# Kernel optimization log

Hardware: AMD Instinct MI355X
Metric: run time of the kernel (lower is better)

The kernel has to match this reference:

```python
import jax, jax.numpy as jnp
import numpy as np

H, HD = 8, 64  # num_heads, head_dim
EPS = 1e-6

def rmsnorm(x, scale):
    return x * jax.lax.rsqrt(jnp.mean(x * x, axis=-1, keepdims=True) + EPS) * scale

def lecun(key, shape):
    fan_in = shape[0]
    return jax.random.normal(key, shape, dtype=jnp.float32) * (fan_in ** -0.5)

def setup_inputs() -> dict:
    key = jax.random.key(0)
    ks = jax.random.split(key, 12)
    B, S, D = 2, 512, 512
    hidden = H * HD            # 512
    ffn = 4 * D                # 2048
    return {
        "inputs": jax.random.normal(ks[0], (B, S, D), dtype=jnp.float32),
        "mask": jnp.zeros((B, S), dtype=jnp.float32),
        "carry": jnp.zeros((B, H, HD, HD), dtype=jnp.float32),
        "ln1": jnp.ones((D,), dtype=jnp.float32),
        "Wq": lecun(ks[1], (D, hidden)),
        "Wk": lecun(ks[2], (D, hidden)),
        "Wv": lecun(ks[3], (D, hidden)),
        "attn_ln": jnp.ones((hidden,), dtype=jnp.float32),
        "Wo": lecun(ks[4], (hidden, D)),
        "bo": jnp.zeros((D,), dtype=jnp.float32),
        "ln2": jnp.ones((D,), dtype=jnp.float32),
        "Wg": lecun(ks[5], (D, ffn)),
        "Wu": lecun(ks[6], (D, ffn)),
        "Wd": lecun(ks[7], (ffn, D)),
    }

def reference(inputs, mask, carry, ln1, Wq, Wk, Wv, attn_ln, Wo, bo, ln2, Wg, Wu, Wd):
    B, S, D = inputs.shape
    skip = inputs
    x = rmsnorm(inputs, ln1)
    # projections + relu feature map
    q = jax.nn.relu((x @ Wq).reshape(B, S, H, HD))
    k = jax.nn.relu((x @ Wk).reshape(B, S, H, HD))
    v = (x @ Wv).reshape(B, S, H, HD)
    # matrix-valued state update: Bmat_t = v_t k_t^T  [B,S,H,HD,HD]
    Bmat = v[..., :, None] * k[..., None, :]
    # decay: identity, zeroed where mask==1 (episode reset)
    m = mask[:, :, None, None, None]
    A = jnp.broadcast_to(jnp.eye(HD, dtype=x.dtype), Bmat.shape) * (1.0 - m)

    def binop(lhs, rhs):
        a_i, b_i = lhs
        a_j, b_j = rhs
        return jnp.matmul(a_i, a_j), jnp.matmul(b_i, a_j) + b_j

    cum_decay, hidden_states = jax.lax.associative_scan(binop, (A, Bmat), axis=1)
    # fold in incoming carry
    states = jnp.matmul(carry[:, None], cum_decay) + hidden_states  # [B,S,H,HD,HD]
    attn = jnp.matmul(states, q[..., None]).squeeze(-1).reshape(B, S, H * HD)
    attn = rmsnorm(attn, attn_ln)
    y = attn @ Wo + bo
    final_carry = states[:, -1]
    # residual + SwiGLU FFN
    x = y + skip
    skip2 = x
    x = rmsnorm(x, ln2)
    x = (jax.nn.silu(x @ Wg) * (x @ Wu)) @ Wd
    return (final_carry, x + skip2)
```

## Files before the change

### kernel.cpp

```cpp
#include <hip/hip_runtime.h>
#include <math.h>

typedef __bf16 bf16x8 __attribute__((ext_vector_type(8)));
typedef float  f32x4  __attribute__((ext_vector_type(4)));

constexpr int B_=2, S_=512, D_=512, H_=8, HD_=64, FFN_=2048, NC_=8;
constexpr float EPS_=1e-6f;

__device__ __forceinline__ __bf16 f2bf(float f){
    union{float f;unsigned u;}x; x.f=f;
    unsigned r=(x.u+0x7fffu+((x.u>>16)&1u))>>16;
    union{unsigned short s;__bf16 b;}y; y.s=(unsigned short)r; return y.b;
}
__device__ __forceinline__ float bf2f(unsigned short s){
    union{unsigned u;float f;}x; x.u=((unsigned)s)<<16; return x.f;
}
__device__ __forceinline__ void bf8_f32(uint4 p, float* o){
    unsigned w[4]={p.x,p.y,p.z,p.w};
#pragma unroll
    for(int i=0;i<4;i++){ o[2*i]=bf2f((unsigned short)(w[i]&0xffffu)); o[2*i+1]=bf2f((unsigned short)(w[i]>>16)); }
}
__device__ __forceinline__ f32x4 MF(bf16x8 a, bf16x8 b, f32x4 c){
    return __builtin_amdgcn_mfma_f32_16x16x32_bf16(a,b,c,0,0,0);
}
#define GLOAD16(g,l) __builtin_amdgcn_global_load_lds((__attribute__((address_space(1))) const void*)(g),(__attribute__((address_space(3))) void*)(l),16,0,0)

__global__ __launch_bounds__(256) void wprep_k(const float* __restrict__ Wg,
    const float* __restrict__ Wu, const float* __restrict__ Wd,
    const float* __restrict__ Wq, const float* __restrict__ Wk,
    const float* __restrict__ Wv, const float* __restrict__ Wo,
    __bf16* __restrict__ WT){
    int t = blockIdx.x;
    const float* src; __bf16* dst; int K,N,lt;
    if      (t<256){ src=Wg; dst=WT;          K=512;  N=2048; lt=t; }
    else if (t<512){ src=Wu; dst=WT+1048576;  K=512;  N=2048; lt=t-256; }
    else if (t<768){ src=Wd; dst=WT+2097152;  K=2048; N=512;  lt=t-512; }
    else if (t<832){ src=Wq; dst=WT+3145728;  K=512;  N=512;  lt=t-768; }
    else if (t<896){ src=Wk; dst=WT+3407872;  K=512;  N=512;  lt=t-832; }
    else if (t<960){ src=Wv; dst=WT+3670016;  K=512;  N=512;  lt=t-896; }
    else           { src=Wo; dst=WT+3932160;  K=512;  N=512;  lt=t-960; }
    int nt64 = N>>6, tk = lt/nt64, tn = lt%nt64;
    __shared__ __bf16 s[64][72];
    int tid = threadIdx.x;
    {
        int jk = tid>>2, jn0 = (tid&3)*16;
        const float* p = src + (size_t)(tk*64+jk)*N + tn*64 + jn0;
        float4 a0=((const float4*)p)[0], a1=((const float4*)p)[1],
               a2=((const float4*)p)[2], a3=((const float4*)p)[3];
        bf16x8 w0, w1;
        w0[0]=f2bf(a0.x); w0[1]=f2bf(a0.y); w0[2]=f2bf(a0.z); w0[3]=f2bf(a0.w);
        w0[4]=f2bf(a1.x); w0[5]=f2bf(a1.y); w0[6]=f2bf(a1.z); w0[7]=f2bf(a1.w);
        w1[0]=f2bf(a2.x); w1[1]=f2bf(a2.y); w1[2]=f2bf(a2.z); w1[3]=f2bf(a2.w);
        w1[4]=f2bf(a3.x); w1[5]=f2bf(a3.y); w1[6]=f2bf(a3.z); w1[7]=f2bf(a3.w);
        *(bf16x8*)&s[jk][jn0] = w0; *(bf16x8*)&s[jk][jn0+8] = w1;
    }
    __syncthreads();
    {
        int jn = tid>>2, jk0 = (tid&3)*16;
        bf16x8 w0, w1;
#pragma unroll
        for(int j=0;j<8;j++){ w0[j]=s[jk0+j][jn]; w1[j]=s[jk0+8+j][jn]; }
        __bf16* q = dst + (size_t)(tn*64+jn)*K + tk*64 + jk0;
        *(bf16x8*)q = w0; *(bf16x8*)(q+8) = w1;
    }
}

__global__ __launch_bounds__(256) void rowrms_f32_k(const float* __restrict__ X, float* __restrict__ rs){
    int row = blockIdx.x*4 + (threadIdx.x>>6), lane = threadIdx.x&63;
    const float4* p = (const float4*)(X + (size_t)row*D_) + lane*2;
    float4 a=p[0], b=p[1];
    float ss = a.x*a.x+a.y*a.y+a.z*a.z+a.w*a.w + b.x*b.x+b.y*b.y+b.z*b.z+b.w*b.w;
    for(int off=32; off>0; off>>=1) ss += __shfl_down(ss, off, 64);
    if(lane==0) rs[row] = rsqrtf(ss/(float)D_ + EPS_);
}
__global__ __launch_bounds__(256) void rowrms_bf16_k(const __bf16* __restrict__ X, float* __restrict__ rs){
    int row = blockIdx.x*4 + (threadIdx.x>>6), lane = threadIdx.x&63;
    uint4 p = *(const uint4*)(X + (size_t)row*D_ + lane*8);
    float v[8]; bf8_f32(p, v);
    float ss = 0.f;
#pragma unroll
    for(int i=0;i<8;i++) ss += v[i]*v[i];
    for(int off=32; off>0; off>>=1) ss += __shfl_down(ss, off, 64);
    if(lane==0) rs[row] = rsqrtf(ss/(float)D_ + EPS_);
}

__device__ __forceinline__ void stageB_async(const __bf16* __restrict__ Bt, int n0, int K, int kk,
                                             __bf16* sB0, __bf16* sB1, int wave, int lane){
    int row = (wave<<4) + (lane>>2), kq = (lane&3)<<3;
    const __bf16* g = Bt + (size_t)(n0+row)*K + kk + kq;
    GLOAD16(g,      sB0 + (wave<<9));
    GLOAD16(g + 32, sB1 + (wave<<9));
}
__device__ __forceinline__ void stageA_rms_f32(const float* __restrict__ A, const float* __restrict__ rs,
        const float* __restrict__ g, int m0, int K, int kk, __bf16* sA0, __bf16* sA1, int tid){
    int row = tid>>2, kq = (tid&3)<<4;
    float r = rs[m0+row];
    const float4* p = (const float4*)(A + (size_t)(m0+row)*K + kk + kq);
    const float4* gp = (const float4*)(g + kk + kq);
    float4 a[4] = {p[0],p[1],p[2],p[3]};
    float4 gg[4] = {gp[0],gp[1],gp[2],gp[3]};
    bf16x8 w0, w1;
    w0[0]=f2bf(a[0].x*r*gg[0].x); w0[1]=f2bf(a[0].y*r*gg[0].y);
    w0[2]=f2bf(a[0].z*r*gg[0].z); w0[3]=f2bf(a[0].w*r*gg[0].w);
    w0[4]=f2bf(a[1].x*r*gg[1].x); w0[5]=f2bf(a[1].y*r*gg[1].y);
    w0[6]=f2bf(a[1].z*r*gg[1].z); w0[7]=f2bf(a[1].w*r*gg[1].w);
    w1[0]=f2bf(a[2].x*r*gg[2].x); w1[1]=f2bf(a[2].y*r*gg[2].y);
    w1[2]=f2bf(a[2].z*r*gg[2].z); w1[3]=f2bf(a[2].w*r*gg[2].w);
    w1[4]=f2bf(a[3].x*r*gg[3].x); w1[5]=f2bf(a[3].y*r*gg[3].y);
    w1[6]=f2bf(a[3].z*r*gg[3].z); w1[7]=f2bf(a[3].w*r*gg[3].w);
    __bf16* d = (kq<32) ? (sA0 + row*32 + kq) : (sA1 + row*32 + kq-32);
    *(bf16x8*)d = w0; *(bf16x8*)(d+8) = w1;
}
__device__ __forceinline__ void stageA_rms_bf16(const __bf16* __restrict__ A, const float* __restrict__ rs,
        const float* __restrict__ g, int m0, int K, int kk, __bf16* sA0, __bf16* sA1, int tid){
    int row = tid>>2, kq = (tid&3)<<4;
    float r = rs[m0+row];
    const __bf16* p = A + (size_t)(m0+row)*K + kk + kq;
    float v[16]; bf8_f32(*(const uint4*)p, v); bf8_f32(*(const uint4*)(p+8), v+8);
    const float4* gp = (const float4*)(g + kk + kq);
    float4 gg[4] = {gp[0],gp[1],gp[2],gp[3]};
    float gf[16] = {gg[0].x,gg[0].y,gg[0].z,gg[0].w, gg[1].x,gg[1].y,gg[1].z,gg[1].w,
                    gg[2].x,gg[2].y,gg[2].z,gg[2].w, gg[3].x,gg[3].y,gg[3].z,gg[3].w};
    bf16x8 w0, w1;
#pragma unroll
    for(int j=0;j<8;j++){ w0[j]=f2bf(v[j]*r*gf[j]); w1[j]=f2bf(v[8+j]*r*gf[8+j]); }
    __bf16* d = (kq<32) ? (sA0 + row*32 + kq) : (sA1 + row*32 + kq-32);
    *(bf16x8*)d = w0; *(bf16x8*)(d+8) = w1;
}
__device__ __forceinline__ void mfma_tile(const __bf16* sA0, const __bf16* sA1,
        const __bf16* sB0, const __bf16* sB1, int wave, int lane, f32x4 acc[4]){
    int ar = (((wave<<4)+(lane&15))<<5) + ((lane>>4)<<3);
    bf16x8 a0 = *(const bf16x8*)(sA0+ar);
    bf16x8 a1 = *(const bf16x8*)(sA1+ar);
#pragma unroll
    for(int nt=0;nt<4;nt++){
        int br = (((nt<<4)+(lane&15))<<5) + ((lane>>4)<<3);
        acc[nt] = MF(a0, *(const bf16x8*)(sB0+br), acc[nt]);
        acc[nt] = MF(a1, *(const bf16x8*)(sB1+br), acc[nt]);
    }
}

__global__ __launch_bounds__(256) void gemm_qkv_k(const float* __restrict__ in,
        const float* __restrict__ rs1, const float* __restrict__ ln1,
        const __bf16* __restrict__ Bt, __bf16* __restrict__ Qb,
        __bf16* __restrict__ Kb, __bf16* __restrict__ Vb){
    __shared__ __bf16 sA0[2048], sA1[2048], sB0[2048], sB1[2048];
    int tid=threadIdx.x, wave=tid>>6, lane=tid&63;
    int n0 = blockIdx.x*64, m0 = blockIdx.y*64;
    f32x4 acc[4] = {};
    for(int kk=0; kk<512; kk+=64){
        stageB_async(Bt, n0, 512, kk, sB0, sB1, wave, lane);
        stageA_rms_f32(in, rs1, ln1, m0, 512, kk, sA0, sA1, tid);
        __syncthreads();
        mfma_tile(sA0,sA1,sB0,sB1,wave,lane,acc);
        __syncthreads();
    }
    int seg = n0>>9, nc = n0&511;
    __bf16* Out = seg==0 ? Qb : (seg==1 ? Kb : Vb);
    bool rl = seg<2;
    int r0 = (wave<<4) + ((lane>>4)<<2);
#pragma unroll
    for(int nt=0;nt<4;nt++){
        int col = nc + nt*16 + (lane&15);
#pragma unroll
        for(int r=0;r<4;r++){
            float v = acc[nt][r]; if(rl) v = fmaxf(v,0.f);
            Out[(size_t)(m0+r0+r)*512 + col] = f2bf(v);
        }
    }
}

__global__ __launch_bounds__(256) void gemm_wo_k(const __bf16* __restrict__ attn,
        const float* __restrict__ rs2, const float* __restrict__ aln,
        const __bf16* __restrict__ Bt, const float* __restrict__ bo,
        const float* __restrict__ skip, float* __restrict__ outx, __bf16* __restrict__ X1){
    __shared__ __bf16 sA0[2048], sA1[2048], sB0[2048], sB1[2048];
    int tid=threadIdx.x, wave=tid>>6, lane=tid&63;
    int n0 = blockIdx.x*64, m0 = blockIdx.y*64;
    f32x4 acc[4] = {};
    for(int kk=0; kk<512; kk+=64){
        stageB_async(Bt, n0, 512, kk, sB0, sB1, wave, lane);
        stageA_rms_bf16(attn, rs2, aln, m0, 512, kk, sA0, sA1, tid);
        __syncthreads();
        mfma_tile(sA0,sA1,sB0,sB1,wave,lane,acc);
        __syncthreads();
    }
    int r0 = (wave<<4) + ((lane>>4)<<2);
#pragma unroll
    for(int nt=0;nt<4;nt++){
        int col = n0 + nt*16 + (lane&15);
#pragma unroll
        for(int r=0;r<4;r++){
            int row = m0+r0+r;
            float v = acc[nt][r] + bo[col] + skip[(size_t)row*512+col];
            outx[(size_t)row*512+col] = v;
            X1[(size_t)row*512+col] = f2bf(v);
        }
    }
}

__global__ __launch_bounds__(256) void gemm_dual_k(const __bf16* __restrict__ X1,
        const float* __restrict__ rs3, const float* __restrict__ ln2,
        const __bf16* __restrict__ Gt, const __bf16* __restrict__ Ut,
        __bf16* __restrict__ Hb){
    __shared__ __bf16 sA0[2048], sA1[2048], sG0[2048], sG1[2048], sU0[2048], sU1[2048];
    int tid=threadIdx.x, wave=tid>>6, lane=tid&63;
    int n0 = blockIdx.x*64, m0 = blockIdx.y*64;
    f32x4 ag[4] = {}, au[4] = {};
    for(int kk=0; kk<512; kk+=64){
        stageB_async(Gt, n0, 512, kk, sG0, sG1, wave, lane);
        stageB_async(Ut, n0, 512, kk, sU0, sU1, wave, lane);
        stageA_rms_bf16(X1, rs3, ln2, m0, 512, kk, sA0, sA1, tid);
        __syncthreads();
        {
            int ar = (((wave<<4)+(lane&15))<<5) + ((lane>>4)<<3);
            bf16x8 a0 = *(const bf16x8*)(sA0+ar);
            bf16x8 a1 = *(const bf16x8*)(sA1+ar);
#pragma unroll
            for(int nt=0;nt<4;nt++){
                int br = (((nt<<4)+(lane&15))<<5) + ((lane>>4)<<3);
                ag[nt] = MF(a0, *(const bf16x8*)(sG0+br), ag[nt]);
                ag[nt] = MF(a1, *(const bf16x8*)(sG1+br), ag[nt]);
                au[nt] = MF(a0, *(const bf16x8*)(sU0+br), au[nt]);
                au[nt] = MF(a1, *(const bf16x8*)(sU1+br), au[nt]);
            }
        }
        __syncthreads();
    }
    int r0 = (wave<<4) + ((lane>>4)<<2);
#pragma unroll
    for(int nt=0;nt<4;nt++){
        int col = n0 + nt*16 + (lane&15);
#pragma unroll
        for(int r=0;r<4;r++){
            float gv = ag[nt][r], uv = au[nt][r];
            float hv = (gv / (1.f + __expf(-gv))) * uv;
            Hb[(size_t)(m0+r0+r)*FFN_ + col] = f2bf(hv);
        }
    }
}

__global__ __launch_bounds__(256) void gemm_wd_k(const __bf16* __restrict__ Hb,
        const __bf16* __restrict__ Bt, float* __restrict__ outx){
    __shared__ __bf16 sA0[2048], sA1[2048], sB0[2048], sB1[2048];
    int tid=threadIdx.x, wave=tid>>6, lane=tid&63;
    int n0 = blockIdx.x*64, m0 = blockIdx.y*64, ks = blockIdx.z*512;
    f32x4 acc[4] = {};
    int row = (wave<<4) + (lane>>2), kq = (lane&3)<<3;
    for(int kk=ks; kk<ks+512; kk+=64){
        stageB_async(Bt, n0, FFN_, kk, sB0, sB1, wave, lane);
        const __bf16* g = Hb + (size_t)(m0+row)*FFN_ + kk + kq;
        GLOAD16(g,      sA0 + (wave<<9));
        GLOAD16(g + 32, sA1 + (wave<<9));
        __syncthreads();
        mfma_tile(sA0,sA1,sB0,sB1,wave,lane,acc);
        __syncthreads();
    }
    int r0 = (wave<<4) + ((lane>>4)<<2);
#pragma unroll
    for(int nt=0;nt<4;nt++){
        int col = n0 + nt*16 + (lane&15);
#pragma unroll
        for(int r=0;r<4;r++)
            atomicAdd(&outx[(size_t)(m0+r0+r)*512 + col], acc[nt][r]);
    }
}

__global__ __launch_bounds__(256) void scanA_k(const __bf16* __restrict__ Kb,
        const __bf16* __restrict__ Vb, const float* __restrict__ mask,
        __bf16* __restrict__ MS, float* __restrict__ Pws){
    int bid = blockIdx.x;
    int c = bid&7, h = (bid>>3)&7, b = bid>>6;
    __shared__ __bf16 sKT0[2048], sKT1[2048], sVT0[2048], sVT1[2048];
    __shared__ float scv[64], ssp[64];
    int tid = threadIdx.x, wave = tid>>6, lane = tid&63;
    const __bf16* Kg = Kb + (size_t)(b*512 + c*64)*512 + h*64;
    const __bf16* Vg = Vb + (size_t)(b*512 + c*64)*512 + h*64;
    if(tid<64) scv[tid] = 1.f - mask[b*512 + c*64 + tid];
    __syncthreads();
    if(tid==0){
        float sp = 1.f;
        for(int t=63;t>=0;--t){ ssp[t]=sp; sp*=scv[t]; }
        Pws[bid] = sp;
    }
    __syncthreads();
#pragma unroll
    for(int p=0;p<2;p++){
        int t = (tid>>3) + p*32, i0 = (tid&7)*8;
        uint4 kr = *(const uint4*)(Kg + (size_t)t*512 + i0);
        uint4 vr = *(const uint4*)(Vg + (size_t)t*512 + i0);
        const __bf16* kp = (const __bf16*)&kr;
        const unsigned short* vp = (const unsigned short*)&vr;
        float sp = ssp[t];
        __bf16* kh = p ? sKT1 : sKT0;
        __bf16* vh = p ? sVT1 : sVT0;
#pragma unroll
        for(int j=0;j<8;j++){
            kh[(i0+j)*32 + (t&31)] = kp[j];
            vh[(i0+j)*32 + (t&31)] = f2bf(bf2f(vp[j])*sp);
        }
    }
    __syncthreads();
    f32x4 am[4] = {};
    mfma_tile(sVT0, sVT1, sKT0, sKT1, wave, lane, am);
    __bf16* Mo = MS + (size_t)bid*4096;
    int r0 = (wave<<4) + ((lane>>4)<<2);
#pragma unroll
    for(int nt=0;nt<4;nt++){
        int j = nt*16 + (lane&15);
#pragma unroll
        for(int r=0;r<4;r++) Mo[(size_t)(r0+r)*64 + j] = f2bf(am[nt][r]);
    }
}

__global__ __launch_bounds__(256) void scanB_k(const float* __restrict__ carry,
        __bf16* __restrict__ MS, const float* __restrict__ Pws,
        float* __restrict__ carry_out){
    int bh = blockIdx.x, tid = threadIdx.x;
    int i = tid>>2, j0 = (tid&3)*16;
    float s[16];
    const float* ci = carry + (size_t)bh*4096 + i*64 + j0;
    for(int j=0;j<16;j++) s[j]=ci[j];
    for(int cc=0; cc<NC_; ++cc){
        __bf16* p = MS + ((size_t)bh*NC_+cc)*4096 + i*64 + j0;
        float P = Pws[bh*NC_+cc];
        for(int j=0;j<16;j++){
            float m = bf2f(*(const unsigned short*)&p[j]);
            p[j] = f2bf(s[j]);
            s[j] = s[j]*P + m;
        }
    }
    float* co = carry_out + (size_t)bh*4096 + i*64 + j0;
    for(int j=0;j<16;j++) co[j]=s[j];
}

__global__ __launch_bounds__(256) void scanC_k(const __bf16* __restrict__ Qb,
        const __bf16* __restrict__ Kb, const __bf16* __restrict__ Vb,
        const float* __restrict__ mask, const __bf16* __restrict__ MS,
        __bf16* __restrict__ attn){
    int bid = blockIdx.x;
    int c = bid&7, h = (bid>>3)&7, b = bid>>6;
    __shared__ __bf16 sQ0[2048], sQ1[2048], sK0[2048], sK1[2048];
    __shared__ __bf16 sS0[2048], sS1[2048];
    __shared__ __bf16 sVT0[2048], sVT1[2048];
    __shared__ __bf16 sW0[2048], sW1[2048];
    __shared__ float Wtab[64][64];
    __shared__ float scv[64], pp[64];
    int tid = threadIdx.x, wave = tid>>6, lane = tid&63;
    const __bf16* Qg = Qb + (size_t)(b*512 + c*64)*512 + h*64;
    const __bf16* Kg = Kb + (size_t)(b*512 + c*64)*512 + h*64;
    const __bf16* Vg = Vb + (size_t)(b*512 + c*64)*512 + h*64;
    const __bf16* Sg = MS + ((size_t)((b*H_+h)*NC_ + c))*4096;

    stageB_async(Qg, 0, 512, 0, sQ0, sQ1, wave, lane);
    stageB_async(Kg, 0, 512, 0, sK0, sK1, wave, lane);
    stageB_async(Sg, 0, 64,  0, sS0, sS1, wave, lane);
    if(tid<64) scv[tid] = 1.f - mask[b*512 + c*64 + tid];
#pragma unroll
    for(int p=0;p<2;p++){
        int u = (tid>>3) + p*32, i0 = (tid&7)*8;
        uint4 vr = *(const uint4*)(Vg + (size_t)u*512 + i0);
        const __bf16* vp = (const __bf16*)&vr;
        __bf16* vh = p ? sVT1 : sVT0;
#pragma unroll
        for(int j=0;j<8;j++) vh[(i0+j)*32 + (u&31)] = vp[j];
    }
    __syncthreads();
    if(tid<64){
        int u = tid; float w = 1.f;
        for(int t=0;t<64;t++){
            if(t>u) w *= scv[t];
            Wtab[u][t] = (t<u) ? 0.f : w;
        }
    }
    if(tid==64){
        float p=1.f;
        for(int t=0;t<64;t++){ p*=scv[t]; pp[t]=p; }
    }
    f32x4 sc[4] = {};
    mfma_tile(sK0, sK1, sQ0, sQ1, wave, lane, sc);
    __syncthreads();
    {
        int u0 = (wave<<4) + ((lane>>4)<<2);
#pragma unroll
        for(int nt=0;nt<4;nt++){
            int t = nt*16 + (lane&15);
#pragma unroll
            for(int r=0;r<4;r++){
                int u = u0 + r;
                float v = sc[nt][r] * Wtab[u][t];
                ((u<32) ? sW0 : sW1)[t*32 + (u&31)] = f2bf(v);
            }
        }
    }
    __syncthreads();
    f32x4 aI[4] = {}, aX[4] = {};
    mfma_tile(sW0, sW1, sVT0, sVT1, wave, lane, aI);
    mfma_tile(sQ0, sQ1, sS0, sS1, wave, lane, aX);
    int t0 = (wave<<4) + ((lane>>4)<<2);
#pragma unroll
    for(int nt=0;nt<4;nt++){
        int i = nt*16 + (lane&15);
#pragma unroll
        for(int r=0;r<4;r++){
            int t = t0 + r;
            float o = aI[nt][r] + aX[nt][r]*pp[t];
            attn[(size_t)(b*512 + c*64 + t)*512 + h*64 + i] = f2bf(o);
        }
    }
}

extern "C" void kernel_launch(void* const* d_in, const int* in_sizes, int n_in,
                              void* d_out, int out_size, void* d_ws, size_t ws_size,
                              hipStream_t stream) {
    const float* inputs  = (const float*)d_in[0];
    const float* mask    = (const float*)d_in[1];
    const float* carry   = (const float*)d_in[2];
    const float* ln1     = (const float*)d_in[3];
    const float* Wq      = (const float*)d_in[4];
    const float* Wk      = (const float*)d_in[5];
    const float* Wv      = (const float*)d_in[6];
    const float* attn_ln = (const float*)d_in[7];
    const float* Wo      = (const float*)d_in[8];
    const float* bo      = (const float*)d_in[9];
    const float* ln2     = (const float*)d_in[10];
    const float* Wg      = (const float*)d_in[11];
    const float* Wu      = (const float*)d_in[12];
    const float* Wd      = (const float*)d_in[13];

    float* out_carry = (float*)d_out;
    float* out_x     = (float*)d_out + 65536;

    __bf16* wb = (__bf16*)d_ws;
    float*  wf = (float*)d_ws;
    __bf16* WgT   = wb;
    __bf16* WuT   = wb + 1048576;
    __bf16* WdT   = wb + 2097152;
    __bf16* WqkvT = wb + 3145728;
    __bf16* WoT   = wb + 3932160;
    __bf16* Qb    = wb + 4194304;
    __bf16* Kb    = wb + 4718592;
    __bf16* Vb    = wb + 5242880;
    __bf16* Hb    = wb + 3145728;
    __bf16* MS    = wb + 5767168;
    float*  Pws   = wf + 3145728;
    float*  rs1   = wf + 3145856;
    float*  rs2   = wf + 3146880;
    float*  rs3   = wf + 3147904;

    wprep_k<<<dim3(1024), dim3(256), 0, stream>>>(Wg,Wu,Wd,Wq,Wk,Wv,Wo, wb);
    rowrms_f32_k<<<dim3(256), dim3(256), 0, stream>>>(inputs, rs1);
    gemm_qkv_k<<<dim3(24,16), dim3(256), 0, stream>>>(inputs, rs1, ln1, WqkvT, Qb, Kb, Vb);
    scanA_k<<<dim3(128), dim3(256), 0, stream>>>(Kb, Vb, mask, MS, Pws);
    scanB_k<<<dim3(16), dim3(256), 0, stream>>>(carry, MS, Pws, out_carry);
    scanC_k<<<dim3(128), dim3(256), 0, stream>>>(Qb, Kb, Vb, mask, MS, Qb);
    rowrms_bf16_k<<<dim3(256), dim3(256), 0, stream>>>(Qb, rs2);
    gemm_wo_k<<<dim3(8,16), dim3(256), 0, stream>>>(Qb, rs2, attn_ln, WoT, bo, inputs, out_x, Vb);
    rowrms_bf16_k<<<dim3(256), dim3(256), 0, stream>>>(Vb, rs3);
    gemm_dual_k<<<dim3(32,16), dim3(256), 0, stream>>>(Vb, rs3, ln2, WgT, WuT, Hb);
    gemm_wd_k<<<dim3(8,16,4), dim3(256), 0, stream>>>(Hb, WdT, out_x);
}
```

Before: 166.0 us.

## Fuse RMS reductions into GEMM epilogues, merge scan stages, widen GEMM N tiles

Removes the standalone row-RMS kernels. rs1 is now computed inside the weight-prep launch, while rs2 and rs3 are built from sum-of-squares atomics in the scanC and Wo epilogues. The sequential scanB carry-propagation kernel is folded into scanC: each chunk block recomputes its prefix state from earlier chunk summaries and the last chunk writes the final carry. All GEMMs widen their N tile from 64 to 128. This cuts four launches but halves grid sizes, which may lower occupancy on a large GPU, and it adds atomics plus redundant prefix work in scanC.

```diff
diff --git a/kernel.cpp b/kernel.cpp
--- a/kernel.cpp
+++ b/kernel.cpp
@@ -25,12 +25,38 @@
 }
 #define GLOAD16(g,l) __builtin_amdgcn_global_load_lds((__attribute__((address_space(1))) const void*)(g),(__attribute__((address_space(3))) void*)(l),16,0,0)
 
-__global__ __launch_bounds__(256) void wprep_k(const float* __restrict__ Wg,
+__device__ __forceinline__ void rowsq_atomic(float* accb, int row0, int lane, float p[4]){
+#pragma unroll
+    for(int r=0;r<4;r++){
+        float v = p[r];
+        v += __shfl_xor(v, 1, 64);
+        v += __shfl_xor(v, 2, 64);
+        v += __shfl_xor(v, 4, 64);
+        v += __shfl_xor(v, 8, 64);
+        if((lane&15)==0) atomicAdd(accb + row0 + r, v);
+    }
+}
+
+__global__ __launch_bounds__(256) void prep_k(const float* __restrict__ Wg,
     const float* __restrict__ Wu, const float* __restrict__ Wd,
     const float* __restrict__ Wq, const float* __restrict__ Wk,
     const float* __restrict__ Wv, const float* __restrict__ Wo,
-    __bf16* __restrict__ WT){
-    int t = blockIdx.x;
+    __bf16* __restrict__ WT, const float* __restrict__ inputs,
+    float* __restrict__ rs1, float* __restrict__ rs2acc, float* __restrict__ rs3acc){
+    __shared__ __bf16 s[64][72];
+    int t = blockIdx.x, tid = threadIdx.x;
+    if(t >= 1024){
+        int row = (t-1024)*4 + (tid>>6), lane = tid&63;
+        const float4* p = (const float4*)(inputs + (size_t)row*D_) + lane*2;
+        float4 a=p[0], b=p[1];
+        float ss = a.x*a.x+a.y*a.y+a.z*a.z+a.w*a.w + b.x*b.x+b.y*b.y+b.z*b.z+b.w*b.w;
+        for(int off=32; off>0; off>>=1) ss += __shfl_down(ss, off, 64);
+        if(lane==0) rs1[row] = rsqrtf(ss/(float)D_ + EPS_);
+        float4 z = {0.f,0.f,0.f,0.f};
+        if(t==1024) ((float4*)rs2acc)[tid] = z;
+        if(t==1025) ((float4*)rs3acc)[tid] = z;
+        return;
+    }
     const float* src; __bf16* dst; int K,N,lt;
     if      (t<256){ src=Wg; dst=WT;          K=512;  N=2048; lt=t; }
     else if (t<512){ src=Wu; dst=WT+1048576;  K=512;  N=2048; lt=t-256; }
@@ -40,8 +66,6 @@
     else if (t<960){ src=Wv; dst=WT+3670016;  K=512;  N=512;  lt=t-896; }
     else           { src=Wo; dst=WT+3932160;  K=512;  N=512;  lt=t-960; }
     int nt64 = N>>6, tk = lt/nt64, tn = lt%nt64;
-    __shared__ __bf16 s[64][72];
-    int tid = threadIdx.x;
     {
         int jk = tid>>2, jn0 = (tid&3)*16;
         const float* p = src + (size_t)(tk*64+jk)*N + tn*64 + jn0;
@@ -65,27 +89,18 @@
     }
 }
 
-__global__ __launch_bounds__(256) void rowrms_f32_k(const float* __restrict__ X, float* __restrict__ rs){
-    int row = blockIdx.x*4 + (threadIdx.x>>6), lane = threadIdx.x&63;
-    const float4* p = (const float4*)(X + (size_t)row*D_) + lane*2;
-    float4 a=p[0], b=p[1];
-    float ss = a.x*a.x+a.y*a.y+a.z*a.z+a.w*a.w + b.x*b.x+b.y*b.y+b.z*b.z+b.w*b.w;
-    for(int off=32; off>0; off>>=1) ss += __shfl_down(ss, off, 64);
-    if(lane==0) rs[row] = rsqrtf(ss/(float)D_ + EPS_);
-}
-__global__ __launch_bounds__(256) void rowrms_bf16_k(const __bf16* __restrict__ X, float* __restrict__ rs){
-    int row = blockIdx.x*4 + (threadIdx.x>>6), lane = threadIdx.x&63;
-    uint4 p = *(const uint4*)(X + (size_t)row*D_ + lane*8);
-    float v[8]; bf8_f32(p, v);
-    float ss = 0.f;
-#pragma unroll
-    for(int i=0;i<8;i++) ss += v[i]*v[i];
-    for(int off=32; off>0; off>>=1) ss += __shfl_down(ss, off, 64);
-    if(lane==0) rs[row] = rsqrtf(ss/(float)D_ + EPS_);
-}
-
-__device__ __forceinline__ void stageB_async(const __bf16* __restrict__ Bt, int n0, int K, int kk,
-                                             __bf16* sB0, __bf16* sB1, int wave, int lane){
+__device__ __forceinline__ void stageB2(const __bf16* __restrict__ Bt, int n0, int K, int kk,
+                                        __bf16* sB0, __bf16* sB1, int wave, int lane){
+    int row = (wave<<4) + (lane>>2), kq = (lane&3)<<3;
+    const __bf16* g = Bt + (size_t)(n0+row)*K + kk + kq;
+    GLOAD16(g,      sB0 + (wave<<9));
+    GLOAD16(g + 32, sB1 + (wave<<9));
+    const __bf16* g2 = g + (size_t)64*K;
+    GLOAD16(g2,      sB0 + 2048 + (wave<<9));
+    GLOAD16(g2 + 32, sB1 + 2048 + (wave<<9));
+}
+__device__ __forceinline__ void stageB1(const __bf16* __restrict__ Bt, int n0, int K, int kk,
+                                        __bf16* sB0, __bf16* sB1, int wave, int lane){
     int row = (wave<<4) + (lane>>2), kq = (lane&3)<<3;
     const __bf16* g = Bt + (size_t)(n0+row)*K + kk + kq;
     GLOAD16(g,      sB0 + (wave<<9));
@@ -111,10 +126,10 @@
     __bf16* d = (kq<32) ? (sA0 + row*32 + kq) : (sA1 + row*32 + kq-32);
     *(bf16x8*)d = w0; *(bf16x8*)(d+8) = w1;
 }
-__device__ __forceinline__ void stageA_rms_bf16(const __bf16* __restrict__ A, const float* __restrict__ rs,
+__device__ __forceinline__ void stageA_rms_acc(const __bf16* __restrict__ A, const float* __restrict__ ssq,
         const float* __restrict__ g, int m0, int K, int kk, __bf16* sA0, __bf16* sA1, int tid){
     int row = tid>>2, kq = (tid&3)<<4;
-    float r = rs[m0+row];
+    float r = rsqrtf(ssq[m0+row]*(1.f/(float)D_) + EPS_);
     const __bf16* p = A + (size_t)(m0+row)*K + kk + kq;
     float v[16]; bf8_f32(*(const uint4*)p, v); bf8_f32(*(const uint4*)(p+8), v+8);
     const float4* gp = (const float4*)(g + kk + kq);
@@ -139,20 +154,32 @@
         acc[nt] = MF(a1, *(const bf16x8*)(sB1+br), acc[nt]);
     }
 }
+__device__ __forceinline__ void mfma_tile8(const __bf16* sA0, const __bf16* sA1,
+        const __bf16* sB0, const __bf16* sB1, int wave, int lane, f32x4 acc[8]){
+    int ar = (((wave<<4)+(lane&15))<<5) + ((lane>>4)<<3);
+    bf16x8 a0 = *(const bf16x8*)(sA0+ar);
+    bf16x8 a1 = *(const bf16x8*)(sA1+ar);
+#pragma unroll
+    for(int nt=0;nt<8;nt++){
+        int br = (((nt<<4)+(lane&15))<<5) + ((lane>>4)<<3);
+        acc[nt] = MF(a0, *(const bf16x8*)(sB0+br), acc[nt]);
+        acc[nt] = MF(a1, *(const bf16x8*)(sB1+br), acc[nt]);
+    }
+}
 
 __global__ __launch_bounds__(256) void gemm_qkv_k(const float* __restrict__ in,
         const float* __restrict__ rs1, const float* __restrict__ ln1,
         const __bf16* __restrict__ Bt, __bf16* __restrict__ Qb,
         __bf16* __restrict__ Kb, __bf16* __restrict__ Vb){
-    __shared__ __bf16 sA0[2048], sA1[2048], sB0[2048], sB1[2048];
+    __shared__ __bf16 sA0[2048], sA1[2048], sB0[4096], sB1[4096];
     int tid=threadIdx.x, wave=tid>>6, lane=tid&63;
-    int n0 = blockIdx.x*64, m0 = blockIdx.y*64;
-    f32x4 acc[4] = {};
+    int n0 = blockIdx.x*128, m0 = blockIdx.y*64;
+    f32x4 acc[8] = {};
     for(int kk=0; kk<512; kk+=64){
-        stageB_async(Bt, n0, 512, kk, sB0, sB1, wave, lane);
+        stageB2(Bt, n0, 512, kk, sB0, sB1, wave, lane);
         stageA_rms_f32(in, rs1, ln1, m0, 512, kk, sA0, sA1, tid);
         __syncthreads();
-        mfma_tile(sA0,sA1,sB0,sB1,wave,lane,acc);
+        mfma_tile8(sA0,sA1,sB0,sB1,wave,lane,acc);
         __syncthreads();
     }
     int seg = n0>>9, nc = n0&511;
@@ -160,109 +187,13 @@
     bool rl = seg<2;
     int r0 = (wave<<4) + ((lane>>4)<<2);
 #pragma unroll
-    for(int nt=0;nt<4;nt++){
+    for(int nt=0;nt<8;nt++){
         int col = nc + nt*16 + (lane&15);
 #pragma unroll
         for(int r=0;r<4;r++){
             float v = acc[nt][r]; if(rl) v = fmaxf(v,0.f);
             Out[(size_t)(m0+r0+r)*512 + col] = f2bf(v);
         }
-    }
-}
-
-__global__ __launch_bounds__(256) void gemm_wo_k(const __bf16* __restrict__ attn,
-        const float* __restrict__ rs2, const float* __restrict__ aln,
-        const __bf16* __restrict__ Bt, const float* __restrict__ bo,
-        const float* __restrict__ skip, float* __restrict__ outx, __bf16* __restrict__ X1){
-    __shared__ __bf16 sA0[2048], sA1[2048], sB0[2048], sB1[2048];
-    int tid=threadIdx.x, wave=tid>>6, lane=tid&63;
-    int n0 = blockIdx.x*64, m0 = blockIdx.y*64;
-    f32x4 acc[4] = {};
-    for(int kk=0; kk<512; kk+=64){
-        stageB_async(Bt, n0, 512, kk, sB0, sB1, wave, lane);
-        stageA_rms_bf16(attn, rs2, aln, m0, 512, kk, sA0, sA1, tid);
-        __syncthreads();
-        mfma_tile(sA0,sA1,sB0,sB1,wave,lane,acc);
-        __syncthreads();
-    }
-    int r0 = (wave<<4) + ((lane>>4)<<2);
-#pragma unroll
-    for(int nt=0;nt<4;nt++){
-        int col = n0 + nt*16 + (lane&15);
-#pragma unroll
-        for(int r=0;r<4;r++){
-            int row = m0+r0+r;
-            float v = acc[nt][r] + bo[col] + skip[(size_t)row*512+col];
-            outx[(size_t)row*512+col] = v;
-            X1[(size_t)row*512+col] = f2bf(v);
-        }
-    }
-}
-
-__global__ __launch_bounds__(256) void gemm_dual_k(const __bf16* __restrict__ X1,
-        const float* __restrict__ rs3, const float* __restrict__ ln2,
-        const __bf16* __restrict__ Gt, const __bf16* __restrict__ Ut,
-        __bf16* __restrict__ Hb){
-    __shared__ __bf16 sA0[2048], sA1[2048], sG0[2048], sG1[2048], sU0[2048], sU1[2048];
-    int tid=threadIdx.x, wave=tid>>6, lane=tid&63;
-    int n0 = blockIdx.x*64, m0 = blockIdx.y*64;
-    f32x4 ag[4] = {}, au[4] = {};
-    for(int kk=0; kk<512; kk+=64){
-        stageB_async(Gt, n0, 512, kk, sG0, sG1, wave, lane);
-        stageB_async(Ut, n0, 512, kk, sU0, sU1, wave, lane);
-        stageA_rms_bf16(X1, rs3, ln2, m0, 512, kk, sA0, sA1, tid);
-        __syncthreads();
-        {
-            int ar = (((wave<<4)+(lane&15))<<5) + ((lane>>4)<<3);
-            bf16x8 a0 = *(const bf16x8*)(sA0+ar);
-            bf16x8 a1 = *(const bf16x8*)(sA1+ar);
-#pragma unroll
-            for(int nt=0;nt<4;nt++){
-                int br = (((nt<<4)+(lane&15))<<5) + ((lane>>4)<<3);
-                ag[nt] = MF(a0, *(const bf16x8*)(sG0+br), ag[nt]);
-                ag[nt] = MF(a1, *(const bf16x8*)(sG1+br), ag[nt]);
-                au[nt] = MF(a0, *(const bf16x8*)(sU0+br), au[nt]);
-                au[nt] = MF(a1, *(const bf16x8*)(sU1+br), au[nt]);
-            }
-        }
-        __syncthreads();
-    }
-    int r0 = (wave<<4) + ((lane>>4)<<2);
-#pragma unroll
-    for(int nt=0;nt<4;nt++){
-        int col = n0 + nt*16 + (lane&15);
-#pragma unroll
-        for(int r=0;r<4;r++){
-            float gv = ag[nt][r], uv = au[nt][r];
-            float hv = (gv / (1.f + __expf(-gv))) * uv;
-            Hb[(size_t)(m0+r0+r)*FFN_ + col] = f2bf(hv);
-        }
-    }
-}
-
-__global__ __launch_bounds__(256) void gemm_wd_k(const __bf16* __restrict__ Hb,
-        const __bf16* __restrict__ Bt, float* __restrict__ outx){
-    __shared__ __bf16 sA0[2048], sA1[2048], sB0[2048], sB1[2048];
-    int tid=threadIdx.x, wave=tid>>6, lane=tid&63;
-    int n0 = blockIdx.x*64, m0 = blockIdx.y*64, ks = blockIdx.z*512;
-    f32x4 acc[4] = {};
-    int row = (wave<<4) + (lane>>2), kq = (lane&3)<<3;
-    for(int kk=ks; kk<ks+512; kk+=64){
-        stageB_async(Bt, n0, FFN_, kk, sB0, sB1, wave, lane);
-        const __bf16* g = Hb + (size_t)(m0+row)*FFN_ + kk + kq;
-        GLOAD16(g,      sA0 + (wave<<9));
-        GLOAD16(g + 32, sA1 + (wave<<9));
-        __syncthreads();
-        mfma_tile(sA0,sA1,sB0,sB1,wave,lane,acc);
-        __syncthreads();
-    }
-    int r0 = (wave<<4) + ((lane>>4)<<2);
-#pragma unroll
-    for(int nt=0;nt<4;nt++){
-        int col = n0 + nt*16 + (lane&15);
-#pragma unroll
-        for(int r=0;r<4;r++)
-            atomicAdd(&outx[(size_t)(m0+r0+r)*512 + col], acc[nt][r]);
     }
 }
 
@@ -313,33 +244,15 @@
     }
 }
 
-__global__ __launch_bounds__(256) void scanB_k(const float* __restrict__ carry,
-        __bf16* __restrict__ MS, const float* __restrict__ Pws,
-        float* __restrict__ carry_out){
-    int bh = blockIdx.x, tid = threadIdx.x;
-    int i = tid>>2, j0 = (tid&3)*16;
-    float s[16];
-    const float* ci = carry + (size_t)bh*4096 + i*64 + j0;
-    for(int j=0;j<16;j++) s[j]=ci[j];
-    for(int cc=0; cc<NC_; ++cc){
-        __bf16* p = MS + ((size_t)bh*NC_+cc)*4096 + i*64 + j0;
-        float P = Pws[bh*NC_+cc];
-        for(int j=0;j<16;j++){
-            float m = bf2f(*(const unsigned short*)&p[j]);
-            p[j] = f2bf(s[j]);
-            s[j] = s[j]*P + m;
-        }
-    }
-    float* co = carry_out + (size_t)bh*4096 + i*64 + j0;
-    for(int j=0;j<16;j++) co[j]=s[j];
-}
-
 __global__ __launch_bounds__(256) void scanC_k(const __bf16* __restrict__ Qb,
         const __bf16* __restrict__ Kb, const __bf16* __restrict__ Vb,
         const float* __restrict__ mask, const __bf16* __restrict__ MS,
-        __bf16* __restrict__ attn){
+        const float* __restrict__ carry, const float* __restrict__ Pws,
+        float* __restrict__ carry_out, __bf16* __restrict__ attn,
+        float* __restrict__ rs2acc){
     int bid = blockIdx.x;
     int c = bid&7, h = (bid>>3)&7, b = bid>>6;
+    int bh = b*H_ + h;
     __shared__ __bf16 sQ0[2048], sQ1[2048], sK0[2048], sK1[2048];
     __shared__ __bf16 sS0[2048], sS1[2048];
     __shared__ __bf16 sVT0[2048], sVT1[2048];
@@ -350,11 +263,9 @@
     const __bf16* Qg = Qb + (size_t)(b*512 + c*64)*512 + h*64;
     const __bf16* Kg = Kb + (size_t)(b*512 + c*64)*512 + h*64;
     const __bf16* Vg = Vb + (size_t)(b*512 + c*64)*512 + h*64;
-    const __bf16* Sg = MS + ((size_t)((b*H_+h)*NC_ + c))*4096;
-
-    stageB_async(Qg, 0, 512, 0, sQ0, sQ1, wave, lane);
-    stageB_async(Kg, 0, 512, 0, sK0, sK1, wave, lane);
-    stageB_async(Sg, 0, 64,  0, sS0, sS1, wave, lane);
+
+    stageB1(Qg, 0, 512, 0, sQ0, sQ1, wave, lane);
+    stageB1(Kg, 0, 512, 0, sK0, sK1, wave, lane);
     if(tid<64) scv[tid] = 1.f - mask[b*512 + c*64 + tid];
 #pragma unroll
     for(int p=0;p<2;p++){
@@ -365,6 +276,39 @@
 #pragma unroll
         for(int j=0;j<8;j++) vh[(i0+j)*32 + (u&31)] = vp[j];
     }
+    {
+        int i = tid>>2, j0 = (tid&3)*16;
+        float s[16];
+        const float* ci = carry + (size_t)bh*4096 + i*64 + j0;
+        const float4* c4 = (const float4*)ci;
+        float4 s4[4] = {c4[0],c4[1],c4[2],c4[3]};
+        float* sp = (float*)s4;
+#pragma unroll
+        for(int j=0;j<16;j++) s[j]=sp[j];
+        for(int cc=0; cc<c; ++cc){
+            float P = Pws[bh*8+cc];
+            const __bf16* mp = MS + ((size_t)bh*8+cc)*4096 + i*64 + j0;
+            float mv[16]; bf8_f32(*(const uint4*)mp, mv); bf8_f32(*(const uint4*)(mp+8), mv+8);
+#pragma unroll
+            for(int j=0;j<16;j++) s[j] = s[j]*P + mv[j];
+        }
+        bf16x8 w0, w1;
+#pragma unroll
+        for(int j=0;j<8;j++){ w0[j]=f2bf(s[j]); w1[j]=f2bf(s[8+j]); }
+        __bf16* d = (j0<32) ? (sS0 + i*32 + j0) : (sS1 + i*32 + j0-32);
+        *(bf16x8*)d = w0; *(bf16x8*)(d+8) = w1;
+        if(c==7){
+            float P = Pws[bh*8+7];
+            const __bf16* mp = MS + ((size_t)bh*8+7)*4096 + i*64 + j0;
+            float mv[16]; bf8_f32(*(const uint4*)mp, mv); bf8_f32(*(const uint4*)(mp+8), mv+8);
+            float4 o4[4];
+            float* ov = (float*)o4;
+#pragma unroll
+            for(int j=0;j<16;j++) ov[j] = s[j]*P + mv[j];
+            float4* co = (float4*)(carry_out + (size_t)bh*4096 + i*64 + j0);
+            co[0]=o4[0]; co[1]=o4[1]; co[2]=o4[2]; co[3]=o4[3];
+        }
+    }
     __syncthreads();
     if(tid<64){
         int u = tid; float w = 1.f;
@@ -398,6 +342,7 @@
     mfma_tile(sW0, sW1, sVT0, sVT1, wave, lane, aI);
     mfma_tile(sQ0, sQ1, sS0, sS1, wave, lane, aX);
     int t0 = (wave<<4) + ((lane>>4)<<2);
+    float psum[4] = {0.f,0.f,0.f,0.f};
 #pragma unroll
     for(int nt=0;nt<4;nt++){
         int i = nt*16 + (lane&15);
@@ -406,7 +351,109 @@
             int t = t0 + r;
             float o = aI[nt][r] + aX[nt][r]*pp[t];
             attn[(size_t)(b*512 + c*64 + t)*512 + h*64 + i] = f2bf(o);
-        }
+            psum[r] += o*o;
+        }
+    }
+    rowsq_atomic(rs2acc, b*512 + c*64 + t0, lane, psum);
+}
+
+__global__ __launch_bounds__(256) void gemm_wo_k(const __bf16* __restrict__ attn,
+        const float* __restrict__ rs2acc, const float* __restrict__ aln,
+        const __bf16* __restrict__ Bt, const float* __restrict__ bo,
+        const float* __restrict__ skip, float* __restrict__ outx,
+        __bf16* __restrict__ X1, float* __restrict__ rs3acc){
+    __shared__ __bf16 sA0[2048], sA1[2048], sB0[4096], sB1[4096];
+    int tid=threadIdx.x, wave=tid>>6, lane=tid&63;
+    int n0 = blockIdx.x*128, m0 = blockIdx.y*64;
+    f32x4 acc[8] = {};
+    for(int kk=0; kk<512; kk+=64){
+        stageB2(Bt, n0, 512, kk, sB0, sB1, wave, lane);
+        stageA_rms_acc(attn, rs2acc, aln, m0, 512, kk, sA0, sA1, tid);
+        __syncthreads();
+        mfma_tile8(sA0,sA1,sB0,sB1,wave,lane,acc);
+        __syncthreads();
+    }
+    int r0 = (wave<<4) + ((lane>>4)<<2);
+    float psum[4] = {0.f,0.f,0.f,0.f};
+#pragma unroll
+    for(int nt=0;nt<8;nt++){
+        int col = n0 + nt*16 + (lane&15);
+#pragma unroll
+        for(int r=0;r<4;r++){
+            int row = m0+r0+r;
+            float v = acc[nt][r] + bo[col] + skip[(size_t)row*512+col];
+            outx[(size_t)row*512+col] = v;
+            X1[(size_t)row*512+col] = f2bf(v);
+            psum[r] += v*v;
+        }
+    }
+    rowsq_atomic(rs3acc, m0+r0, lane, psum);
+}
+
+__global__ __launch_bounds__(256) void gemm_dual_k(const __bf16* __restrict__ X1,
+        const float* __restrict__ rs3acc, const float* __restrict__ ln2,
+        const __bf16* __restrict__ Gt, const __bf16* __restrict__ Ut,
+        __bf16* __restrict__ Hb){
+    __shared__ __bf16 sA0[2048], sA1[2048], sG0[4096], sG1[4096], sU0[4096], sU1[4096];
+    int tid=threadIdx.x, wave=tid>>6, lane=tid&63;
+    int n0 = blockIdx.x*128, m0 = blockIdx.y*64;
+    f32x4 ag[8] = {}, au[8] = {};
+    for(int kk=0; kk<512; kk+=64){
+        stageB2(Gt, n0, 512, kk, sG0, sG1, wave, lane);
+        stageB2(Ut, n0, 512, kk, sU0, sU1, wave, lane);
+        stageA_rms_acc(X1, rs3acc, ln2, m0, 512, kk, sA0, sA1, tid);
+        __syncthreads();
+        {
+            int ar = (((wave<<4)+(lane&15))<<5) + ((lane>>4)<<3);
+            bf16x8 a0 = *(const bf16x8*)(sA0+ar);
+            bf16x8 a1 = *(const bf16x8*)(sA1+ar);
+#pragma unroll
+            for(int nt=0;nt<8;nt++){
+                int br = (((nt<<4)+(lane&15))<<5) + ((lane>>4)<<3);
+                ag[nt] = MF(a0, *(const bf16x8*)(sG0+br), ag[nt]);
+                ag[nt] = MF(a1, *(const bf16x8*)(sG1+br), ag[nt]);
+                au[nt] = MF(a0, *(const bf16x8*)(sU0+br), au[nt]);
+                au[nt] = MF(a1, *(const bf16x8*)(sU1+br), au[nt]);
+            }
+        }
+        __syncthreads();
+    }
+    int r0 = (wave<<4) + ((lane>>4)<<2);
+#pragma unroll
+    for(int nt=0;nt<8;nt++){
+        int col = n0 + nt*16 + (lane&15);
+#pragma unroll
+        for(int r=0;r<4;r++){
+            float gv = ag[nt][r], uv = au[nt][r];
+            float hv = (gv / (1.f + __expf(-gv))) * uv;
+            Hb[(size_t)(m0+r0+r)*FFN_ + col] = f2bf(hv);
+        }
+    }
+}
+
+__global__ __launch_bounds__(256) void gemm_wd_k(const __bf16* __restrict__ Hb,
+        const __bf16* __restrict__ Bt, float* __restrict__ outx){
+    __shared__ __bf16 sA0[2048], sA1[2048], sB0[4096], sB1[4096];
+    int tid=threadIdx.x, wave=tid>>6, lane=tid&63;
+    int n0 = blockIdx.x*128, m0 = blockIdx.y*64, ks = blockIdx.z*512;
+    f32x4 acc[8] = {};
+    int row = (wave<<4) + (lane>>2), kq = (lane&3)<<3;
+    for(int kk=ks; kk<ks+512; kk+=64){
+        stageB2(Bt, n0, FFN_, kk, sB0, sB1, wave, lane);
+        const __bf16* g = Hb + (size_t)(m0+row)*FFN_ + kk + kq;
+        GLOAD16(g,      sA0 + (wave<<9));
+        GLOAD16(g + 32, sA1 + (wave<<9));
+        __syncthreads();
+        mfma_tile8(sA0,sA1,sB0,sB1,wave,lane,acc);
+        __syncthreads();
+    }
+    int r0 = (wave<<4) + ((lane>>4)<<2);
+#pragma unroll
+    for(int nt=0;nt<8;nt++){
+        int col = n0 + nt*16 + (lane&15);
+#pragma unroll
+        for(int r=0;r<4;r++)
+            atomicAdd(&outx[(size_t)(m0+r0+r)*512 + col], acc[nt][r]);
     }
 }
 
@@ -445,18 +492,14 @@
     __bf16* MS    = wb + 5767168;
     float*  Pws   = wf + 3145728;
     float*  rs1   = wf + 3145856;
-    float*  rs2   = wf + 3146880;
-    float*  rs3   = wf + 3147904;
-
-    wprep_k<<<dim3(1024), dim3(256), 0, stream>>>(Wg,Wu,Wd,Wq,Wk,Wv,Wo, wb);
-    rowrms_f32_k<<<dim3(256), dim3(256), 0, stream>>>(inputs, rs1);
-    gemm_qkv_k<<<dim3(24,16), dim3(256), 0, stream>>>(inputs, rs1, ln1, WqkvT, Qb, Kb, Vb);
+    float*  rs2a  = wf + 3146880;
+    float*  rs3a  = wf + 3147904;
+
+    prep_k<<<dim3(1280), dim3(256), 0, stream>>>(Wg,Wu,Wd,Wq,Wk,Wv,Wo, wb, inputs, rs1, rs2a, rs3a);
+    gemm_qkv_k<<<dim3(12,16), dim3(256), 0, stream>>>(inputs, rs1, ln1, WqkvT, Qb, Kb, Vb);
     scanA_k<<<dim3(128), dim3(256), 0, stream>>>(Kb, Vb, mask, MS, Pws);
-    scanB_k<<<dim3(16), dim3(256), 0, stream>>>(carry, MS, Pws, out_carry);
-    scanC_k<<<dim3(128), dim3(256), 0, stream>>>(Qb, Kb, Vb, mask, MS, Qb);
-    rowrms_bf16_k<<<dim3(256), dim3(256), 0, stream>>>(Qb, rs2);
-    gemm_wo_k<<<dim3(8,16), dim3(256), 0, stream>>>(Qb, rs2, attn_ln, WoT, bo, inputs, out_x, Vb);
-    rowrms_bf16_k<<<dim3(256), dim3(256), 0, stream>>>(Vb, rs3);
-    gemm_dual_k<<<dim3(32,16), dim3(256), 0, stream>>>(Vb, rs3, ln2, WgT, WuT, Hb);
-    gemm_wd_k<<<dim3(8,16,4), dim3(256), 0, stream>>>(Hb, WdT, out_x);
-}
+    scanC_k<<<dim3(128), dim3(256), 0, stream>>>(Qb, Kb, Vb, mask, MS, carry, Pws, out_carry, Qb, rs2a);
+    gemm_wo_k<<<dim3(4,16), dim3(256), 0, stream>>>(Qb, rs2a, attn_ln, WoT, bo, inputs, out_x, Vb, rs3a);
+    gemm_dual_k<<<dim3(16,16), dim3(256), 0, stream>>>(Vb, rs3a, ln2, WgT, WuT, Hb);
+    gemm_wd_k<<<dim3(4,16,4), dim3(256), 0, stream>>>(Hb, WdT, out_x);
+}
```

Result: slower. 169.9 us (+2.3%).
